# Optimization experiments

Measured on AMD Instinct MI355X. Metric: run time of the kernel, lower is better.

The kernel has to match this reference:

```python
import jax, jax.numpy as jnp
import numpy as np

DEPTH = 4
N_MOLS = 2000
ATOMS_PER_MOL = 50
N_ATOMS = N_MOLS * ATOMS_PER_MOL + 1   # +1 zero-padding row (chemprop convention)
N_BONDS = 200001                        # +1 zero-padding row
MAX_NB = 6
ATOM_FDIM, BOND_FDIM, HIDDEN = 133, 147, 300


def setup_inputs() -> dict:
    key = jax.random.key(0)
    ks = jax.random.split(key, 12)
    f_atoms = jax.random.uniform(ks[0], (N_ATOMS, ATOM_FDIM), jnp.float32).at[0].set(0.0)
    f_bonds = jax.random.uniform(ks[1], (N_BONDS, BOND_FDIM), jnp.float32).at[0].set(0.0)
    w_atoms = jax.random.uniform(ks[2], (N_ATOMS,), jnp.float32) + 0.5
    w_bonds = (jax.random.uniform(ks[3], (N_BONDS,), jnp.float32) + 0.5).at[0].set(0.0)
    a2b = jax.random.randint(ks[4], (N_ATOMS, MAX_NB), 0, N_BONDS, jnp.int32)
    b2a = jax.random.randint(ks[5], (N_BONDS,), 0, N_ATOMS, jnp.int32)
    b2revb = jax.random.randint(ks[6], (N_BONDS,), 0, N_BONDS, jnp.int32)
    # segment id per atom; padding atom 0 -> dummy segment N_MOLS (dropped)
    mol_id = jnp.concatenate([jnp.array([N_MOLS], jnp.int32),
                              jnp.repeat(jnp.arange(N_MOLS, dtype=jnp.int32), ATOMS_PER_MOL)])
    degree_of_polym = jax.random.uniform(ks[7], (N_MOLS,), jnp.float32) + 0.5
    s = 0.05
    W_i = jax.random.normal(ks[8], (BOND_FDIM, HIDDEN), jnp.float32) * s
    W_h = jax.random.normal(ks[9], (HIDDEN, HIDDEN), jnp.float32) * s
    W_o = jax.random.normal(ks[10], (ATOM_FDIM + HIDDEN, HIDDEN), jnp.float32) * s
    b_o = jnp.zeros((HIDDEN,), jnp.float32)
    return dict(f_atoms=f_atoms, f_bonds=f_bonds, w_atoms=w_atoms, w_bonds=w_bonds,
                degree_of_polym=degree_of_polym, W_i=W_i, W_h=W_h, W_o=W_o, b_o=b_o,
                a2b=a2b, b2a=b2a, b2revb=b2revb, mol_id=mol_id)


def reference(f_atoms, f_bonds, w_atoms, w_bonds, degree_of_polym,
              W_i, W_h, W_o, b_o, a2b, b2a, b2revb, mol_id):
    # bond-message MPNN (atom_messages=False, undirected=False, ReLU, dropout=0 eval)
    inp = f_bonds @ W_i                                   # [n_bonds, H], no bias
    message = jax.nn.relu(inp)
    for _ in range(DEPTH - 1):
        # gather incoming directed-bond messages per atom and weight them
        nei_msg = message[a2b] * w_bonds[a2b][..., None]  # [n_atoms, max_nb, H]
        a_message = nei_msg.sum(axis=1)                   # [n_atoms, H]
        # subtract reverse message (weighted)
        message = a_message[b2a] - message[b2revb] * w_bonds[:, None]
        message = jax.nn.relu(inp + message @ W_h)
    # final atom aggregation
    nei_msg = message[a2b] * w_bonds[a2b][..., None]
    a_message = nei_msg.sum(axis=1)                       # [n_atoms, H]
    a_input = jnp.concatenate([f_atoms, a_message], axis=1)
    atom_hiddens = jax.nn.relu(a_input @ W_o + b_o)       # [n_atoms, H]
    # per-molecule weighted mean readout, scaled by degree of polymerization
    weighted = w_atoms[:, None] * atom_hiddens
    sums = jax.ops.segment_sum(weighted, mol_id, num_segments=N_MOLS + 1)[:N_MOLS]
    wsum = jax.ops.segment_sum(w_atoms, mol_id, num_segments=N_MOLS + 1)[:N_MOLS]
    mol_vecs = degree_of_polym[:, None] * (sums / wsum[:, None])
    return mol_vecs
```

## Files before the change

kernel.cpp:

```cpp
#include <hip/hip_runtime.h>

#define N_MOLS  2000
#define APM     50
#define N_ATOMS 100001
#define N_BONDS 200001
#define MAX_NB  6
#define AF      133
#define BF      147
#define H       300

#define SB    320
#define SF    160
#define MB_P  200192
#define MA_P  100096
#define SWH   320
#define SWI   160
#define SWO   480

typedef _Float16 f16x8 __attribute__((ext_vector_type(8)));
typedef _Float16 f16x4 __attribute__((ext_vector_type(4)));
typedef float    f32x4 __attribute__((ext_vector_type(4)));
typedef float    f32x2 __attribute__((ext_vector_type(2)));

__global__ void cast_fb_kernel(const float* __restrict__ src, _Float16* __restrict__ dst) {
    unsigned i = blockIdx.x * blockDim.x + threadIdx.x;
    if (i >= (unsigned)MB_P * SF) return;
    unsigned m = i / SF, k = i % SF;
    dst[i] = (_Float16)((m < N_BONDS && k < BF) ? src[(size_t)m * BF + k] : 0.f);
}
__global__ void cast_fa_kernel(const float* __restrict__ src, _Float16* __restrict__ dst) {
    unsigned i = blockIdx.x * blockDim.x + threadIdx.x;
    if (i >= (unsigned)MA_P * SF) return;
    unsigned m = i / SF, k = i % SF;
    dst[i] = (_Float16)((m < N_ATOMS && k < AF) ? src[(size_t)m * AF + k] : 0.f);
}
__global__ void cast_wh_kernel(const float* __restrict__ W, _Float16* __restrict__ Wt) {
    int i = blockIdx.x * blockDim.x + threadIdx.x;
    if (i >= 320 * SWH) return;
    const int e = i & 7, quad = (i >> 3) & 3, r16 = (i >> 5) & 15;
    const int rest = i >> 9, ctg = rest % 20, kc = rest / 20;
    const int n = ctg * 16 + r16, k = kc * 32 + quad * 8 + e;
    Wt[i] = (_Float16)((n < H && k < H) ? W[k * H + n] : 0.f);
}
__global__ void cast_wi_kernel(const float* __restrict__ W, _Float16* __restrict__ Wt) {
    int i = blockIdx.x * blockDim.x + threadIdx.x;
    if (i >= 320 * SWI) return;
    const int e = i & 7, quad = (i >> 3) & 3, r16 = (i >> 5) & 15;
    const int rest = i >> 9, ctg = rest % 20, kc = rest / 20;
    const int n = ctg * 16 + r16, k = kc * 32 + quad * 8 + e;
    Wt[i] = (_Float16)((n < H && k < BF) ? W[k * H + n] : 0.f);
}
__global__ void cast_wo_kernel(const float* __restrict__ W, _Float16* __restrict__ Wt) {
    int i = blockIdx.x * blockDim.x + threadIdx.x;
    if (i >= 320 * SWO) return;
    const int e = i & 7, quad = (i >> 3) & 3, r16 = (i >> 5) & 15;
    const int rest = i >> 9, ctg = rest % 20, kc = rest / 20;
    const int n = ctg * 16 + r16, k = kc * 32 + quad * 8 + e;
    float v = 0.f;
    if (n < H) {
        if (k < 320) { if (k < H) v = W[(AF + k) * H + n]; }
        else         { int rr = k - 320; if (rr < AF) v = W[rr * H + n]; }
    }
    Wt[i] = (_Float16)v;
}

template<int NCHUNK, int MODE>
__global__ __launch_bounds__(256, 2) void dgemm_kernel(
    const _Float16* __restrict__ A1, const _Float16* __restrict__ A2,
    const _Float16* __restrict__ Wt, const float* __restrict__ bias,
    _Float16* __restrict__ out16, unsigned char* __restrict__ out8)
{
    __shared__ __align__(16) _Float16 stage[32 * 324];

    const int tid  = threadIdx.x;
    const int lane = tid & 63, wave = tid >> 6;
    const int r16  = lane & 15, quad = lane >> 4;
    const int rowhalf = wave >> 1, colhalf = wave & 1;
    const int row0 = blockIdx.x * 128 + rowhalf * 64;
    const int colb = colhalf * 160;

    f32x4 acc[4][10];
    #pragma unroll
    for (int s = 0; s < 4; ++s)
        #pragma unroll
        for (int ct = 0; ct < 10; ++ct) acc[s][ct] = f32x4{0.f, 0.f, 0.f, 0.f};

    const _Float16* wb = Wt + (size_t)colhalf * 10 * 512 + (r16 * 4 + quad) * 8;

    #pragma unroll
    for (int kc = 0; kc < NCHUNK; ++kc) {
        const _Float16* ap; int kl, sa;
        if (MODE == 2 && kc >= 10) { ap = A2; kl = kc - 10; sa = SF; }
        else                       { ap = A1; kl = kc; sa = (MODE == 0 ? SF : SB); }
        f16x8 a[4];
        #pragma unroll
        for (int s = 0; s < 4; ++s)
            a[s] = *(const f16x8*)(ap + (size_t)(row0 + s * 16 + r16) * sa + kl * 32 + quad * 8);
        #pragma unroll
        for (int ct = 0; ct < 10; ++ct) {
            const f16x8 b = *(const f16x8*)(wb + (size_t)(kc * 20 + ct) * 512);
            #pragma unroll
            for (int s = 0; s < 4; ++s)
                acc[s][ct] = __builtin_amdgcn_mfma_f32_16x16x32_f16(a[s], b, acc[s][ct], 0, 0, 0);
        }
    }

    #pragma unroll
    for (int p = 0; p < 4; ++p) {
        if ((p >> 1) == rowhalf) {
            const int sb0 = (p & 1) * 2;
            #pragma unroll
            for (int s2 = 0; s2 < 2; ++s2) {
                const int s = sb0 + s2;
                #pragma unroll
                for (int ct = 0; ct < 10; ++ct) {
                    const int col = colb + ct * 16 + r16;
                    const float bv = (MODE == 2 && col < H) ? bias[col] : 0.f;
                    const int lr = s2 * 16 + quad * 4;
                    #pragma unroll
                    for (int e = 0; e < 4; ++e)
                        stage[(lr + e) * 324 + col] = (_Float16)(acc[s][ct][e] + bv);
                }
            }
        }
        __syncthreads();
        #pragma unroll
        for (int i = 0; i < 5; ++i) {
            const int c = tid + i * 256;
            const int row = c / 40, colc = (c % 40) * 8;
            const _Float16* sp = stage + row * 324 + colc;
            const f16x4 vlo = *(const f16x4*)(sp);
            const f16x4 vhi = *(const f16x4*)(sp + 4);
            f16x8 v;
            #pragma unroll
            for (int j = 0; j < 4; ++j) { v[j] = vlo[j]; v[j + 4] = vhi[j]; }
            const size_t off = (size_t)(blockIdx.x * 128 + p * 32 + row) * SB + colc;
            if (MODE == 0) {
                float f[8];
                #pragma unroll
                for (int j = 0; j < 8; ++j) f[j] = (float)v[j];
                int w0 = __builtin_amdgcn_cvt_pk_fp8_f32(f[0], f[1], 0, false);
                w0 = __builtin_amdgcn_cvt_pk_fp8_f32(f[2], f[3], w0, true);
                int w1 = __builtin_amdgcn_cvt_pk_fp8_f32(f[4], f[5], 0, false);
                w1 = __builtin_amdgcn_cvt_pk_fp8_f32(f[6], f[7], w1, true);
                uint2 pk; pk.x = (unsigned int)w0; pk.y = (unsigned int)w1;
                *(uint2*)(out8 + off) = pk;
            }
            if (MODE == 0 || MODE == 2) {
                #pragma unroll
                for (int j = 0; j < 8; ++j)
                    v[j] = (v[j] > (_Float16)0) ? v[j] : (_Float16)0;
            }
            *(f16x8*)(out16 + off) = v;
        }
        if (p < 3) __syncthreads();
    }
}

__global__ __launch_bounds__(256, 8) void aggregate_kernel(
    const _Float16* __restrict__ src,
    const int* __restrict__ a2b,
    const float* __restrict__ w_bonds,
    _Float16* __restrict__ dst)
{
    const int lane = threadIdx.x & 63;
    const int a = blockIdx.x * 4 + (threadIdx.x >> 6);
    if (a >= N_ATOMS || lane >= 40) return;
    const int h0 = lane * 8;
    float acc[8] = {0, 0, 0, 0, 0, 0, 0, 0};
    #pragma unroll
    for (int k = 0; k < MAX_NB; ++k) {
        const int b = a2b[a * MAX_NB + k];
        const float w = w_bonds[b];
        const f16x8 m = *(const f16x8*)(src + (size_t)b * SB + h0);
        #pragma unroll
        for (int j = 0; j < 8; ++j) acc[j] += w * (float)m[j];
    }
    f16x8 o;
    #pragma unroll
    for (int j = 0; j < 8; ++j) o[j] = (_Float16)acc[j];
    *(f16x8*)(dst + (size_t)a * SB + h0) = o;
}

__global__ __launch_bounds__(256, 8) void update_kernel(
    const unsigned char* __restrict__ inp8,
    const _Float16* __restrict__ hm,
    const _Float16* __restrict__ hb,
    const int* __restrict__ b2a,
    const int* __restrict__ b2revb,
    const float* __restrict__ w_bonds,
    _Float16* __restrict__ msg)
{
    const int lane = threadIdx.x & 63;
    const int b = blockIdx.x * 4 + (threadIdx.x >> 6);
    if (b >= MB_P || lane >= 40) return;
    const bool real = b < N_BONDS;
    const int bc = real ? b : 0;
    const int a  = b2a[bc];
    const int rb = b2revb[bc];
    const float w = w_bonds[bc];
    const int h0 = lane * 8;
    const uint2 i8  = *(const uint2*)(inp8 + (size_t)b * SB + h0);
    const f16x8 hmv = *(const f16x8*)(hm + (size_t)a  * SB + h0);
    const f16x8 hbv = *(const f16x8*)(hb + (size_t)rb * SB + h0);
    const f32x2 d0 = __builtin_amdgcn_cvt_pk_f32_fp8(i8.x, false);
    const f32x2 d1 = __builtin_amdgcn_cvt_pk_f32_fp8(i8.x, true);
    const f32x2 d2 = __builtin_amdgcn_cvt_pk_f32_fp8(i8.y, false);
    const f32x2 d3 = __builtin_amdgcn_cvt_pk_f32_fp8(i8.y, true);
    const float inpf[8] = {d0[0], d0[1], d1[0], d1[1], d2[0], d2[1], d3[0], d3[1]};
    f16x8 o;
    #pragma unroll
    for (int j = 0; j < 8; ++j) {
        const float v = inpf[j] + (float)hmv[j] - w * (float)hbv[j];
        o[j] = (_Float16)((real && v > 0.f) ? v : 0.f);
    }
    *(f16x8*)(msg + (size_t)b * SB + h0) = o;
}

__global__ __launch_bounds__(256, 8) void readout_kernel(
    const _Float16* __restrict__ ah,
    const float* __restrict__ w_atoms,
    const float* __restrict__ dop,
    float* __restrict__ out)
{
    const int lane = threadIdx.x & 63;
    const int m = blockIdx.x * 4 + (threadIdx.x >> 6);
    if (m >= N_MOLS || lane >= 40) return;
    const int h0 = lane * 8;
    const int a0 = 1 + m * APM;
    float acc[8] = {0, 0, 0, 0, 0, 0, 0, 0};
    float wsum = 0.f;
    for (int i = 0; i < APM; ++i) {
        const float w = w_atoms[a0 + i];
        wsum += w;
        const f16x8 v = *(const f16x8*)(ah + (size_t)(a0 + i) * SB + h0);
        #pragma unroll
        for (int j = 0; j < 8; ++j) acc[j] += w * (float)v[j];
    }
    const float s = dop[m] / wsum;
    #pragma unroll
    for (int j = 0; j < 8; ++j) {
        const int h = h0 + j;
        if (h < H) out[(size_t)m * H + h] = s * acc[j];
    }
}

extern "C" void kernel_launch(void* const* d_in, const int* in_sizes, int n_in,
                              void* d_out, int out_size, void* d_ws, size_t ws_size,
                              hipStream_t stream) {
    const float* f_atoms = (const float*)d_in[0];
    const float* f_bonds = (const float*)d_in[1];
    const float* w_atoms = (const float*)d_in[2];
    const float* w_bonds = (const float*)d_in[3];
    const float* dop     = (const float*)d_in[4];
    const float* W_i     = (const float*)d_in[5];
    const float* W_h     = (const float*)d_in[6];
    const float* W_o     = (const float*)d_in[7];
    const float* b_o     = (const float*)d_in[8];
    const int* a2b    = (const int*)d_in[9];
    const int* b2a    = (const int*)d_in[10];
    const int* b2revb = (const int*)d_in[11];
    float* out = (float*)d_out;

    char* p = (char*)d_ws;
    auto alloc = [&](size_t bytes) {
        char* q = p;
        p += ((bytes + 64 + 255) / 256) * 256;
        return q;
    };
    unsigned char* inp8 = (unsigned char*)alloc((size_t)MB_P * SB);
    _Float16* msg  = (_Float16*)alloc((size_t)MB_P * SB * 2);
    _Float16* hb   = (_Float16*)alloc((size_t)MB_P * SB * 2);
    _Float16* hm   = (_Float16*)alloc((size_t)MA_P * SB * 2);
    _Float16* Wth  = (_Float16*)alloc((size_t)320 * SWH * 2);
    _Float16* Wti  = (_Float16*)alloc((size_t)320 * SWI * 2);
    _Float16* Wto  = (_Float16*)alloc((size_t)320 * SWO * 2);
    _Float16* fb16 = hb;
    _Float16* fa16 = (_Float16*)inp8;
    _Float16* ah   = hb;

    if ((size_t)(p - (char*)d_ws) > ws_size) {
        hipMemsetAsync(d_out, 0, (size_t)out_size * sizeof(float), stream);
        return;
    }

    {
        unsigned n1 = (unsigned)MB_P * SF;
        cast_fb_kernel<<<(n1 + 255) / 256, 256, 0, stream>>>(f_bonds, fb16);
        cast_wh_kernel<<<(320 * SWH + 255) / 256, 256, 0, stream>>>(W_h, Wth);
        cast_wi_kernel<<<(320 * SWI + 255) / 256, 256, 0, stream>>>(W_i, Wti);
        cast_wo_kernel<<<(320 * SWO + 255) / 256, 256, 0, stream>>>(W_o, Wto);
    }

    const int gB = MB_P / 128;
    const int gA = MA_P / 128;
    const int aggGrid = (N_ATOMS + 3) / 4;
    const int updGrid = MB_P / 4;

    dgemm_kernel<5, 0><<<gB, 256, 0, stream>>>(fb16, nullptr, Wti, nullptr, msg, inp8);
    for (int d = 0; d < 3; ++d) {
        dgemm_kernel<10, 1><<<gB, 256, 0, stream>>>(msg, nullptr, Wth, nullptr, hb, nullptr);
        aggregate_kernel<<<aggGrid, 256, 0, stream>>>(hb, a2b, w_bonds, hm);
        update_kernel<<<updGrid, 256, 0, stream>>>(inp8, hm, hb, b2a, b2revb, w_bonds, msg);
    }
    aggregate_kernel<<<aggGrid, 256, 0, stream>>>(msg, a2b, w_bonds, hm);
    {
        unsigned n2 = (unsigned)MA_P * SF;
        cast_fa_kernel<<<(n2 + 255) / 256, 256, 0, stream>>>(f_atoms, fa16);
    }
    dgemm_kernel<15, 2><<<gA, 256, 0, stream>>>(hm, fa16, Wto, b_o, ah, nullptr);
    readout_kernel<<<(N_MOLS + 3) / 4, 256, 0, stream>>>(ah, w_atoms, dop, out);
}
```

Baseline: 1.237 ms.

## Fuse bond message update into the W_h GEMM A-operand load

Adds a GEMM mode that builds each A tile on the fly from the fp8 input projection, the gathered atom aggregate and the reverse-bond message, applying ReLU before the MFMA. This removes the separate update kernel and its full message write and re-read for two of the three depth iterations, and ping-pongs between two bond buffers. In exchange, the GEMM's A loads become irregular gathers repeated for every column half, plus extra conversion ALU work inside the main loop, which may reduce GEMM efficiency.

```diff
diff --git a/kernel.cpp b/kernel.cpp
--- a/kernel.cpp
+++ b/kernel.cpp
@@ -68,7 +68,10 @@
 __global__ __launch_bounds__(256, 2) void dgemm_kernel(
     const _Float16* __restrict__ A1, const _Float16* __restrict__ A2,
     const _Float16* __restrict__ Wt, const float* __restrict__ bias,
-    _Float16* __restrict__ out16, unsigned char* __restrict__ out8)
+    _Float16* __restrict__ out16, unsigned char* __restrict__ out8,
+    const unsigned char* __restrict__ inp8_p,
+    const int* __restrict__ b2a_p, const int* __restrict__ b2revb_p,
+    const float* __restrict__ wb_p)
 {
     __shared__ __align__(16) _Float16 stage[32 * 324];
 
@@ -85,17 +88,53 @@
         #pragma unroll
         for (int ct = 0; ct < 10; ++ct) acc[s][ct] = f32x4{0.f, 0.f, 0.f, 0.f};
 
+    int aidx[4], rbidx[4], rowc[4];
+    float wv[4];
+    bool realb[4];
+    if constexpr (MODE == 3) {
+        #pragma unroll
+        for (int s = 0; s < 4; ++s) {
+            const int row = row0 + s * 16 + r16;
+            realb[s] = row < N_BONDS;
+            rowc[s]  = realb[s] ? row : 0;
+            aidx[s]  = b2a_p[rowc[s]];
+            rbidx[s] = b2revb_p[rowc[s]];
+            wv[s]    = wb_p[rowc[s]];
+        }
+    }
+
     const _Float16* wb = Wt + (size_t)colhalf * 10 * 512 + (r16 * 4 + quad) * 8;
 
     #pragma unroll
     for (int kc = 0; kc < NCHUNK; ++kc) {
-        const _Float16* ap; int kl, sa;
-        if (MODE == 2 && kc >= 10) { ap = A2; kl = kc - 10; sa = SF; }
-        else                       { ap = A1; kl = kc; sa = (MODE == 0 ? SF : SB); }
         f16x8 a[4];
-        #pragma unroll
-        for (int s = 0; s < 4; ++s)
-            a[s] = *(const f16x8*)(ap + (size_t)(row0 + s * 16 + r16) * sa + kl * 32 + quad * 8);
+        if constexpr (MODE == 3) {
+            const int off_h = kc * 32 + quad * 8;
+            #pragma unroll
+            for (int s = 0; s < 4; ++s) {
+                const uint2 i8  = *(const uint2*)(inp8_p + (size_t)rowc[s] * SB + off_h);
+                const f16x8 hmv = *(const f16x8*)(A2 + (size_t)aidx[s]  * SB + off_h);
+                const f16x8 hbv = *(const f16x8*)(A1 + (size_t)rbidx[s] * SB + off_h);
+                const f32x2 d0 = __builtin_amdgcn_cvt_pk_f32_fp8(i8.x, false);
+                const f32x2 d1 = __builtin_amdgcn_cvt_pk_f32_fp8(i8.x, true);
+                const f32x2 d2 = __builtin_amdgcn_cvt_pk_f32_fp8(i8.y, false);
+                const f32x2 d3 = __builtin_amdgcn_cvt_pk_f32_fp8(i8.y, true);
+                const float inpf[8] = {d0[0], d0[1], d1[0], d1[1], d2[0], d2[1], d3[0], d3[1]};
+                #pragma unroll
+                for (int j = 0; j < 8; ++j) {
+                    float v = inpf[j] + (float)hmv[j] - wv[s] * (float)hbv[j];
+                    v = (realb[s] && v > 0.f) ? v : 0.f;
+                    a[s][j] = (_Float16)v;
+                }
+            }
+        } else {
+            const _Float16* ap; int kl, sa;
+            if (MODE == 2 && kc >= 10) { ap = A2; kl = kc - 10; sa = SF; }
+            else                       { ap = A1; kl = kc; sa = (MODE == 0 ? SF : SB); }
+            #pragma unroll
+            for (int s = 0; s < 4; ++s)
+                a[s] = *(const f16x8*)(ap + (size_t)(row0 + s * 16 + r16) * sa + kl * 32 + quad * 8);
+        }
         #pragma unroll
         for (int ct = 0; ct < 10; ++ct) {
             const f16x8 b = *(const f16x8*)(wb + (size_t)(kc * 20 + ct) * 512);
@@ -269,15 +308,15 @@
         return q;
     };
     unsigned char* inp8 = (unsigned char*)alloc((size_t)MB_P * SB);
-    _Float16* msg  = (_Float16*)alloc((size_t)MB_P * SB * 2);
-    _Float16* hb   = (_Float16*)alloc((size_t)MB_P * SB * 2);
+    _Float16* bufX = (_Float16*)alloc((size_t)MB_P * SB * 2);
+    _Float16* bufY = (_Float16*)alloc((size_t)MB_P * SB * 2);
     _Float16* hm   = (_Float16*)alloc((size_t)MA_P * SB * 2);
     _Float16* Wth  = (_Float16*)alloc((size_t)320 * SWH * 2);
     _Float16* Wti  = (_Float16*)alloc((size_t)320 * SWI * 2);
     _Float16* Wto  = (_Float16*)alloc((size_t)320 * SWO * 2);
-    _Float16* fb16 = hb;
+    _Float16* fb16 = bufY;
     _Float16* fa16 = (_Float16*)inp8;
-    _Float16* ah   = hb;
+    _Float16* ah   = bufY;
 
     if ((size_t)(p - (char*)d_ws) > ws_size) {
         hipMemsetAsync(d_out, 0, (size_t)out_size * sizeof(float), stream);
@@ -297,17 +336,24 @@
     const int aggGrid = (N_ATOMS + 3) / 4;
     const int updGrid = MB_P / 4;
 
-    dgemm_kernel<5, 0><<<gB, 256, 0, stream>>>(fb16, nullptr, Wti, nullptr, msg, inp8);
-    for (int d = 0; d < 3; ++d) {
-        dgemm_kernel<10, 1><<<gB, 256, 0, stream>>>(msg, nullptr, Wth, nullptr, hb, nullptr);
-        aggregate_kernel<<<aggGrid, 256, 0, stream>>>(hb, a2b, w_bonds, hm);
-        update_kernel<<<updGrid, 256, 0, stream>>>(inp8, hm, hb, b2a, b2revb, w_bonds, msg);
-    }
-    aggregate_kernel<<<aggGrid, 256, 0, stream>>>(msg, a2b, w_bonds, hm);
+    dgemm_kernel<5, 0><<<gB, 256, 0, stream>>>(fb16, nullptr, Wti, nullptr, bufX, inp8,
+                                               nullptr, nullptr, nullptr, nullptr);
+    dgemm_kernel<10, 1><<<gB, 256, 0, stream>>>(bufX, nullptr, Wth, nullptr, bufY, nullptr,
+                                                nullptr, nullptr, nullptr, nullptr);
+    aggregate_kernel<<<aggGrid, 256, 0, stream>>>(bufY, a2b, w_bonds, hm);
+    dgemm_kernel<10, 3><<<gB, 256, 0, stream>>>(bufY , hm , Wth, nullptr, bufX, nullptr,
+                                                inp8, b2a, b2revb, w_bonds);
+    aggregate_kernel<<<aggGrid, 256, 0, stream>>>(bufX, a2b, w_bonds, hm);
+    dgemm_kernel<10, 3><<<gB, 256, 0, stream>>>(bufX , hm , Wth, nullptr, bufY, nullptr,
+                                                inp8, b2a, b2revb, w_bonds);
+    aggregate_kernel<<<aggGrid, 256, 0, stream>>>(bufY, a2b, w_bonds, hm);
+    update_kernel<<<updGrid, 256, 0, stream>>>(inp8, hm, bufY, b2a, b2revb, w_bonds, bufX);
+    aggregate_kernel<<<aggGrid, 256, 0, stream>>>(bufX, a2b, w_bonds, hm);
     {
         unsigned n2 = (unsigned)MA_P * SF;
         cast_fa_kernel<<<(n2 + 255) / 256, 256, 0, stream>>>(f_atoms, fa16);
     }
-    dgemm_kernel<15, 2><<<gA, 256, 0, stream>>>(hm, fa16, Wto, b_o, ah, nullptr);
+    dgemm_kernel<15, 2><<<gA, 256, 0, stream>>>(hm, fa16, Wto, b_o, ah, nullptr,
+                                                nullptr, nullptr, nullptr, nullptr);
     readout_kernel<<<(N_MOLS + 3) / 4, 256, 0, stream>>>(ah, w_atoms, dop, out);
 }
```

Result: slower. 1.452 ms (+17.4%).

## Fuse bond message update into following W_h GEMM prologue

Applied to the files above, without the earlier changes.

Adds a fused kernel that computes the per-bond update (inp + a_message[b2a] - w*hb[b2revb], ReLU) directly into shared memory and then runs the W_h MFMA GEMM on it. Two of the three update+GEMM pairs are replaced by this kernel, with buffers ping-ponged, so the intermediate message is no longer written to and re-read from global memory. In exchange the kernel uses 64-row tiles with 128 threads and a large LDS tile, which may reduce occupancy and W_h reuse compared with the 128-row GEMM, and the gathers now stall the GEMM prologue.

```diff
diff --git a/kernel.cpp b/kernel.cpp
--- a/kernel.cpp
+++ b/kernel.cpp
@@ -154,6 +154,108 @@
             *(f16x8*)(out16 + off) = v;
         }
         if (p < 3) __syncthreads();
+    }
+}
+
+__global__ __launch_bounds__(128) void dgemm_fused_kernel(
+    const _Float16* __restrict__ hbp,
+    const _Float16* __restrict__ hmp,
+    const unsigned char* __restrict__ inp8,
+    const _Float16* __restrict__ Wt,
+    const int* __restrict__ b2a, const int* __restrict__ b2revb,
+    const float* __restrict__ w_bonds,
+    _Float16* __restrict__ out16)
+{
+    __shared__ __align__(16) _Float16 Als[64 * 336];
+
+    const int tid  = threadIdx.x;
+    const int lane = tid & 63, wave = tid >> 6;
+    const int r16  = lane & 15, quad = lane >> 4;
+    const int row0 = blockIdx.x * 64;
+
+    #pragma unroll 4
+    for (int i = 0; i < 32; ++i) {
+        const int r = wave * 32 + i;
+        const int b = row0 + r;
+        if (lane < 40) {
+            const bool real = b < N_BONDS;
+            const int bc = real ? b : 0;
+            const int a  = b2a[bc];
+            const int rb = b2revb[bc];
+            const float w = w_bonds[bc];
+            const int h0 = lane * 8;
+            const uint2 i8  = *(const uint2*)(inp8 + (size_t)b * SB + h0);
+            const f16x8 hmv = *(const f16x8*)(hmp + (size_t)a  * SB + h0);
+            const f16x8 hbv = *(const f16x8*)(hbp + (size_t)rb * SB + h0);
+            const f32x2 d0 = __builtin_amdgcn_cvt_pk_f32_fp8(i8.x, false);
+            const f32x2 d1 = __builtin_amdgcn_cvt_pk_f32_fp8(i8.x, true);
+            const f32x2 d2 = __builtin_amdgcn_cvt_pk_f32_fp8(i8.y, false);
+            const f32x2 d3 = __builtin_amdgcn_cvt_pk_f32_fp8(i8.y, true);
+            const float inpf[8] = {d0[0], d0[1], d1[0], d1[1], d2[0], d2[1], d3[0], d3[1]};
+            f16x8 o;
+            #pragma unroll
+            for (int j = 0; j < 8; ++j) {
+                const float v = inpf[j] + (float)hmv[j] - w * (float)hbv[j];
+                o[j] = (_Float16)((real && v > 0.f) ? v : 0.f);
+            }
+            *(f16x8*)(&Als[r * 336 + h0]) = o;
+        }
+    }
+    __syncthreads();
+
+    f32x4 acc[4][10];
+    #pragma unroll
+    for (int s = 0; s < 4; ++s)
+        #pragma unroll
+        for (int ct = 0; ct < 10; ++ct) acc[s][ct] = f32x4{0.f, 0.f, 0.f, 0.f};
+
+    const _Float16* wb = Wt + (size_t)wave * 10 * 512 + (r16 * 4 + quad) * 8;
+
+    #pragma unroll
+    for (int kc = 0; kc < 10; ++kc) {
+        f16x8 a[4];
+        #pragma unroll
+        for (int s = 0; s < 4; ++s)
+            a[s] = *(const f16x8*)(&Als[(s * 16 + r16) * 336 + kc * 32 + quad * 8]);
+        #pragma unroll
+        for (int ct = 0; ct < 10; ++ct) {
+            const f16x8 b = *(const f16x8*)(wb + (size_t)(kc * 20 + ct) * 512);
+            #pragma unroll
+            for (int s = 0; s < 4; ++s)
+                acc[s][ct] = __builtin_amdgcn_mfma_f32_16x16x32_f16(a[s], b, acc[s][ct], 0, 0, 0);
+        }
+    }
+    __syncthreads();
+
+    _Float16* stage = Als;
+    #pragma unroll
+    for (int p = 0; p < 2; ++p) {
+        #pragma unroll
+        for (int s2 = 0; s2 < 2; ++s2) {
+            const int s = p * 2 + s2;
+            #pragma unroll
+            for (int ct = 0; ct < 10; ++ct) {
+                const int col = wave * 160 + ct * 16 + r16;
+                const int lr = s2 * 16 + quad * 4;
+                #pragma unroll
+                for (int e = 0; e < 4; ++e)
+                    stage[(lr + e) * 324 + col] = (_Float16)acc[s][ct][e];
+            }
+        }
+        __syncthreads();
+        #pragma unroll
+        for (int i = 0; i < 10; ++i) {
+            const int c = tid + i * 128;
+            const int row = c / 40, colc = (c % 40) * 8;
+            const _Float16* sp = stage + row * 324 + colc;
+            const f16x4 vlo = *(const f16x4*)(sp);
+            const f16x4 vhi = *(const f16x4*)(sp + 4);
+            f16x8 v;
+            #pragma unroll
+            for (int j = 0; j < 4; ++j) { v[j] = vlo[j]; v[j + 4] = vhi[j]; }
+            *(f16x8*)(out16 + (size_t)(row0 + p * 32 + row) * SB + colc) = v;
+        }
+        if (p < 1) __syncthreads();
     }
 }
 
@@ -293,16 +395,19 @@
     }
 
     const int gB = MB_P / 128;
+    const int gF = MB_P / 64;
     const int gA = MA_P / 128;
     const int aggGrid = (N_ATOMS + 3) / 4;
     const int updGrid = MB_P / 4;
 
     dgemm_kernel<5, 0><<<gB, 256, 0, stream>>>(fb16, nullptr, Wti, nullptr, msg, inp8);
-    for (int d = 0; d < 3; ++d) {
-        dgemm_kernel<10, 1><<<gB, 256, 0, stream>>>(msg, nullptr, Wth, nullptr, hb, nullptr);
-        aggregate_kernel<<<aggGrid, 256, 0, stream>>>(hb, a2b, w_bonds, hm);
-        update_kernel<<<updGrid, 256, 0, stream>>>(inp8, hm, hb, b2a, b2revb, w_bonds, msg);
-    }
+    dgemm_kernel<10, 1><<<gB, 256, 0, stream>>>(msg, nullptr, Wth, nullptr, hb, nullptr);
+    aggregate_kernel<<<aggGrid, 256, 0, stream>>>(hb, a2b, w_bonds, hm);
+    dgemm_fused_kernel<<<gF, 128, 0, stream>>>(hb, hm, inp8, Wth, b2a, b2revb, w_bonds, msg);
+    aggregate_kernel<<<aggGrid, 256, 0, stream>>>(msg, a2b, w_bonds, hm);
+    dgemm_fused_kernel<<<gF, 128, 0, stream>>>(msg, hm, inp8, Wth, b2a, b2revb, w_bonds, hb);
+    aggregate_kernel<<<aggGrid, 256, 0, stream>>>(hb, a2b, w_bonds, hm);
+    update_kernel<<<updGrid, 256, 0, stream>>>(inp8, hm, hb, b2a, b2revb, w_bonds, msg);
     aggregate_kernel<<<aggGrid, 256, 0, stream>>>(msg, a2b, w_bonds, hm);
     {
         unsigned n2 = (unsigned)MA_P * SF;
```

New measurement: 1.533 ms. 23.9% more time.

## Store bond messages in FP8 and decode inside GEMM and aggregation

Applied to the files above, without the earlier changes.

The bond message buffer now holds FP8 instead of FP16. The update kernel encodes its output to FP8, the W_h GEMM decodes FP8 operands on load, and a new aggregate8 kernel reads FP8 messages for the final atom aggregation. The first W_h GEMM reads the FP8 pre-activation input directly and applies ReLU while decoding, so the initial GEMM no longer writes a separate FP16 message buffer. This halves the bytes moved for message reads and writes on the bond-sized arrays, at the cost of FP8 precision on intermediate messages and extra per-element conversion work in the GEMM's A-load path.

```diff
diff --git a/kernel.cpp b/kernel.cpp
--- a/kernel.cpp
+++ b/kernel.cpp
@@ -21,6 +21,22 @@
 typedef _Float16 f16x4 __attribute__((ext_vector_type(4)));
 typedef float    f32x4 __attribute__((ext_vector_type(4)));
 typedef float    f32x2 __attribute__((ext_vector_type(2)));
+
+__device__ inline void fp8x8_dec(const uint2 u, float* f) {
+    const f32x2 d0 = __builtin_amdgcn_cvt_pk_f32_fp8(u.x, false);
+    const f32x2 d1 = __builtin_amdgcn_cvt_pk_f32_fp8(u.x, true);
+    const f32x2 d2 = __builtin_amdgcn_cvt_pk_f32_fp8(u.y, false);
+    const f32x2 d3 = __builtin_amdgcn_cvt_pk_f32_fp8(u.y, true);
+    f[0]=d0[0]; f[1]=d0[1]; f[2]=d1[0]; f[3]=d1[1];
+    f[4]=d2[0]; f[5]=d2[1]; f[6]=d3[0]; f[7]=d3[1];
+}
+__device__ inline uint2 fp8x8_enc(const float* f) {
+    int w0 = __builtin_amdgcn_cvt_pk_fp8_f32(f[0], f[1], 0, false);
+    w0 = __builtin_amdgcn_cvt_pk_fp8_f32(f[2], f[3], w0, true);
+    int w1 = __builtin_amdgcn_cvt_pk_fp8_f32(f[4], f[5], 0, false);
+    w1 = __builtin_amdgcn_cvt_pk_fp8_f32(f[6], f[7], w1, true);
+    uint2 r; r.x = (unsigned)w0; r.y = (unsigned)w1; return r;
+}
 
 __global__ void cast_fb_kernel(const float* __restrict__ src, _Float16* __restrict__ dst) {
     unsigned i = blockIdx.x * blockDim.x + threadIdx.x;
@@ -67,6 +83,7 @@
 template<int NCHUNK, int MODE>
 __global__ __launch_bounds__(256, 2) void dgemm_kernel(
     const _Float16* __restrict__ A1, const _Float16* __restrict__ A2,
+    const unsigned char* __restrict__ A8,
     const _Float16* __restrict__ Wt, const float* __restrict__ bias,
     _Float16* __restrict__ out16, unsigned char* __restrict__ out8)
 {
@@ -89,13 +106,28 @@
 
     #pragma unroll
     for (int kc = 0; kc < NCHUNK; ++kc) {
-        const _Float16* ap; int kl, sa;
-        if (MODE == 2 && kc >= 10) { ap = A2; kl = kc - 10; sa = SF; }
-        else                       { ap = A1; kl = kc; sa = (MODE == 0 ? SF : SB); }
         f16x8 a[4];
-        #pragma unroll
-        for (int s = 0; s < 4; ++s)
-            a[s] = *(const f16x8*)(ap + (size_t)(row0 + s * 16 + r16) * sa + kl * 32 + quad * 8);
+        if constexpr (MODE == 4 || MODE == 5) {
+            #pragma unroll
+            for (int s = 0; s < 4; ++s) {
+                const uint2 u = *(const uint2*)(A8 + (size_t)(row0 + s * 16 + r16) * 320 + kc * 32 + quad * 8);
+                float f[8];
+                fp8x8_dec(u, f);
+                #pragma unroll
+                for (int j = 0; j < 8; ++j) {
+                    float v = f[j];
+                    if (MODE == 4) v = v > 0.f ? v : 0.f;
+                    a[s][j] = (_Float16)v;
+                }
+            }
+        } else {
+            const _Float16* ap; int kl, sa;
+            if (MODE == 2 && kc >= 10) { ap = A2; kl = kc - 10; sa = SF; }
+            else                       { ap = A1; kl = kc; sa = (MODE == 0 ? SF : SB); }
+            #pragma unroll
+            for (int s = 0; s < 4; ++s)
+                a[s] = *(const f16x8*)(ap + (size_t)(row0 + s * 16 + r16) * sa + kl * 32 + quad * 8);
+        }
         #pragma unroll
         for (int ct = 0; ct < 10; ++ct) {
             const f16x8 b = *(const f16x8*)(wb + (size_t)(kc * 20 + ct) * 512);
@@ -139,19 +171,15 @@
                 float f[8];
                 #pragma unroll
                 for (int j = 0; j < 8; ++j) f[j] = (float)v[j];
-                int w0 = __builtin_amdgcn_cvt_pk_fp8_f32(f[0], f[1], 0, false);
-                w0 = __builtin_amdgcn_cvt_pk_fp8_f32(f[2], f[3], w0, true);
-                int w1 = __builtin_amdgcn_cvt_pk_fp8_f32(f[4], f[5], 0, false);
-                w1 = __builtin_amdgcn_cvt_pk_fp8_f32(f[6], f[7], w1, true);
-                uint2 pk; pk.x = (unsigned int)w0; pk.y = (unsigned int)w1;
-                *(uint2*)(out8 + off) = pk;
+                *(uint2*)(out8 + off) = fp8x8_enc(f);
+            } else {
+                if (MODE == 2) {
+                    #pragma unroll
+                    for (int j = 0; j < 8; ++j)
+                        v[j] = (v[j] > (_Float16)0) ? v[j] : (_Float16)0;
+                }
+                *(f16x8*)(out16 + off) = v;
             }
-            if (MODE == 0 || MODE == 2) {
-                #pragma unroll
-                for (int j = 0; j < 8; ++j)
-                    v[j] = (v[j] > (_Float16)0) ? v[j] : (_Float16)0;
-            }
-            *(f16x8*)(out16 + off) = v;
         }
         if (p < 3) __syncthreads();
     }
@@ -175,6 +203,33 @@
         const f16x8 m = *(const f16x8*)(src + (size_t)b * SB + h0);
         #pragma unroll
         for (int j = 0; j < 8; ++j) acc[j] += w * (float)m[j];
+    }
+    f16x8 o;
+    #pragma unroll
+    for (int j = 0; j < 8; ++j) o[j] = (_Float16)acc[j];
+    *(f16x8*)(dst + (size_t)a * SB + h0) = o;
+}
+
+__global__ __launch_bounds__(256, 8) void aggregate8_kernel(
+    const unsigned char* __restrict__ src,
+    const int* __restrict__ a2b,
+    const float* __restrict__ w_bonds,
+    _Float16* __restrict__ dst)
+{
+    const int lane = threadIdx.x & 63;
+    const int a = blockIdx.x * 4 + (threadIdx.x >> 6);
+    if (a >= N_ATOMS || lane >= 40) return;
+    const int h0 = lane * 8;
+    float acc[8] = {0, 0, 0, 0, 0, 0, 0, 0};
+    #pragma unroll
+    for (int k = 0; k < MAX_NB; ++k) {
+        const int b = a2b[a * MAX_NB + k];
+        const float w = w_bonds[b];
+        const uint2 u = *(const uint2*)(src + (size_t)b * 320 + h0);
+        float f[8];
+        fp8x8_dec(u, f);
+        #pragma unroll
+        for (int j = 0; j < 8; ++j) acc[j] += w * f[j];
     }
     f16x8 o;
     #pragma unroll
@@ -189,7 +244,7 @@
     const int* __restrict__ b2a,
     const int* __restrict__ b2revb,
     const float* __restrict__ w_bonds,
-    _Float16* __restrict__ msg)
+    unsigned char* __restrict__ msg8)
 {
     const int lane = threadIdx.x & 63;
     const int b = blockIdx.x * 4 + (threadIdx.x >> 6);
@@ -200,21 +255,18 @@
     const int rb = b2revb[bc];
     const float w = w_bonds[bc];
     const int h0 = lane * 8;
-    const uint2 i8  = *(const uint2*)(inp8 + (size_t)b * SB + h0);
+    const uint2 i8  = *(const uint2*)(inp8 + (size_t)b * 320 + h0);
     const f16x8 hmv = *(const f16x8*)(hm + (size_t)a  * SB + h0);
     const f16x8 hbv = *(const f16x8*)(hb + (size_t)rb * SB + h0);
-    const f32x2 d0 = __builtin_amdgcn_cvt_pk_f32_fp8(i8.x, false);
-    const f32x2 d1 = __builtin_amdgcn_cvt_pk_f32_fp8(i8.x, true);
-    const f32x2 d2 = __builtin_amdgcn_cvt_pk_f32_fp8(i8.y, false);
-    const f32x2 d3 = __builtin_amdgcn_cvt_pk_f32_fp8(i8.y, true);
-    const float inpf[8] = {d0[0], d0[1], d1[0], d1[1], d2[0], d2[1], d3[0], d3[1]};
-    f16x8 o;
+    float inpf[8];
+    fp8x8_dec(i8, inpf);
+    float o[8];
     #pragma unroll
     for (int j = 0; j < 8; ++j) {
         const float v = inpf[j] + (float)hmv[j] - w * (float)hbv[j];
-        o[j] = (_Float16)((real && v > 0.f) ? v : 0.f);
-    }
-    *(f16x8*)(msg + (size_t)b * SB + h0) = o;
+        o[j] = (real && v > 0.f) ? v : 0.f;
+    }
+    *(uint2*)(msg8 + (size_t)b * 320 + h0) = fp8x8_enc(o);
 }
 
 __global__ __launch_bounds__(256, 8) void readout_kernel(
@@ -268,8 +320,8 @@
         p += ((bytes + 64 + 255) / 256) * 256;
         return q;
     };
-    unsigned char* inp8 = (unsigned char*)alloc((size_t)MB_P * SB);
-    _Float16* msg  = (_Float16*)alloc((size_t)MB_P * SB * 2);
+    unsigned char* inp8 = (unsigned char*)alloc((size_t)MB_P * 320);
+    unsigned char* msg8 = (unsigned char*)alloc((size_t)MB_P * 320);
     _Float16* hb   = (_Float16*)alloc((size_t)MB_P * SB * 2);
     _Float16* hm   = (_Float16*)alloc((size_t)MA_P * SB * 2);
     _Float16* Wth  = (_Float16*)alloc((size_t)320 * SWH * 2);
@@ -297,17 +349,21 @@
     const int aggGrid = (N_ATOMS + 3) / 4;
     const int updGrid = MB_P / 4;
 
-    dgemm_kernel<5, 0><<<gB, 256, 0, stream>>>(fb16, nullptr, Wti, nullptr, msg, inp8);
-    for (int d = 0; d < 3; ++d) {
-        dgemm_kernel<10, 1><<<gB, 256, 0, stream>>>(msg, nullptr, Wth, nullptr, hb, nullptr);
-        aggregate_kernel<<<aggGrid, 256, 0, stream>>>(hb, a2b, w_bonds, hm);
-        update_kernel<<<updGrid, 256, 0, stream>>>(inp8, hm, hb, b2a, b2revb, w_bonds, msg);
-    }
-    aggregate_kernel<<<aggGrid, 256, 0, stream>>>(msg, a2b, w_bonds, hm);
+    dgemm_kernel<5, 0><<<gB, 256, 0, stream>>>(fb16, nullptr, nullptr, Wti, nullptr, nullptr, inp8);
+    dgemm_kernel<10, 4><<<gB, 256, 0, stream>>>(nullptr, nullptr, inp8, Wth, nullptr, hb, nullptr);
+    aggregate_kernel<<<aggGrid, 256, 0, stream>>>(hb, a2b, w_bonds, hm);
+    update_kernel<<<updGrid, 256, 0, stream>>>(inp8, hm, hb, b2a, b2revb, w_bonds, msg8);
+    dgemm_kernel<10, 5><<<gB, 256, 0, stream>>>(nullptr, nullptr, msg8, Wth, nullptr, hb, nullptr);
+    aggregate_kernel<<<aggGrid, 256, 0, stream>>>(hb, a2b, w_bonds, hm);
+    update_kernel<<<updGrid, 256, 0, stream>>>(inp8, hm, hb, b2a, b2revb, w_bonds, msg8);
+    dgemm_kernel<10, 5><<<gB, 256, 0, stream>>>(nullptr, nullptr, msg8, Wth, nullptr, hb, nullptr);
+    aggregate_kernel<<<aggGrid, 256, 0, stream>>>(hb, a2b, w_bonds, hm);
+    update_kernel<<<updGrid, 256, 0, stream>>>(inp8, hm, hb, b2a, b2revb, w_bonds, msg8);
+    aggregate8_kernel<<<aggGrid, 256, 0, stream>>>(msg8, a2b, w_bonds, hm);
     {
         unsigned n2 = (unsigned)MA_P * SF;
         cast_fa_kernel<<<(n2 + 255) / 256, 256, 0, stream>>>(f_atoms, fa16);
     }
-    dgemm_kernel<15, 2><<<gA, 256, 0, stream>>>(hm, fa16, Wto, b_o, ah, nullptr);
+    dgemm_kernel<15, 2><<<gA, 256, 0, stream>>>(hm, fa16, nullptr, Wto, b_o, ah, nullptr);
     readout_kernel<<<(N_MOLS + 3) / 4, 256, 0, stream>>>(ah, w_atoms, dop, out);
 }
```

After: 1.137 ms. 1.09x faster.
